# Kernel tuning notes

Measured on AMD Instinct MI355X. Metric: run time of the kernel, lower is better.

## Reference

```python
import jax, jax.numpy as jnp
import numpy as np

E = 1024      # embed_dim
H = 16        # num_heads
HD = E // H   # head_dim = 64
R = 8         # dora rank
T, B = 2048, 2


def setup_inputs() -> dict:
    key = jax.random.key(0)
    ks = jax.random.split(key, 16)
    query = jax.random.normal(ks[0], (T, B, E), dtype=jnp.float32)
    kk = jax.random.normal(ks[1], (T, B, E), dtype=jnp.float32)
    vv = jax.random.normal(ks[2], (T, B, E), dtype=jnp.float32)

    def make_dora(k1, k2, k3, k4):
        w = jax.random.normal(k1, (E, E), dtype=jnp.float32) * (E ** -0.5)
        m = jnp.linalg.norm(w)            # magnitude scalar (Frobenius norm)
        V = w / m                          # frozen direction, ||V||_F = 1
        A = jax.random.normal(k2, (R, E), dtype=jnp.float32) * (E ** -0.5)
        Bm = jax.random.normal(k3, (E, R), dtype=jnp.float32) * 0.01
        b = jax.random.normal(k4, (E,), dtype=jnp.float32) * 0.01
        return m, V, A, Bm, b

    mag_q, dir_q, A_q, B_q, bias_q = make_dora(ks[3], ks[4], ks[5], ks[6])
    mag_v, dir_v, A_v, B_v, bias_v = make_dora(ks[7], ks[8], ks[9], ks[10])
    k_w = jax.random.normal(ks[11], (E, E), dtype=jnp.float32) * (E ** -0.5)
    k_b = jax.random.normal(ks[12], (E,), dtype=jnp.float32) * 0.01
    out_w = jax.random.normal(ks[13], (E, E), dtype=jnp.float32) * (E ** -0.5)
    out_b = jax.random.normal(ks[14], (E,), dtype=jnp.float32) * 0.01
    return dict(query=query, key=kk, value=vv,
                mag_q=mag_q, dir_q=dir_q, A_q=A_q, B_q=B_q, bias_q=bias_q,
                mag_v=mag_v, dir_v=dir_v, A_v=A_v, B_v=B_v, bias_v=bias_v,
                k_w=k_w, k_b=k_b, out_w=out_w, out_b=out_b)


def _dora_linear(x, m, V, A, Bm, b):
    # W_eff = m * (V + B@A) / (||V + B@A||_F + 1e-8); out = x @ W_eff.T + b
    Vu = V + Bm @ A                      # [E, E]
    W = (m / (jnp.linalg.norm(Vu) + 1e-8)) * Vu
    return x @ W.T + b


def reference(query, key, value, mag_q, dir_q, A_q, B_q, bias_q,
              mag_v, dir_v, A_v, B_v, bias_v, k_w, k_b, out_w, out_b):
    # NOTE: source module ignores `key`/`value` and derives k, v from `query`.
    Tq, Bq, _ = query.shape
    q = _dora_linear(query, mag_q, dir_q, A_q, B_q, bias_q)   # [T, B, E]
    k = query @ k_w.T + k_b                                    # frozen K proj
    v = _dora_linear(query, mag_v, dir_v, A_v, B_v, bias_v)
    # (T, B, E) -> (B*H, T, HD), matching torch reshape/transpose
    q = q.reshape(Tq, Bq * H, HD).transpose(1, 0, 2)
    k = k.reshape(Tq, Bq * H, HD).transpose(1, 0, 2)
    v = v.reshape(Tq, Bq * H, HD).transpose(1, 0, 2)
    scale = HD ** -0.5
    attn = jnp.einsum('nqd,nkd->nqk', q, k) * scale            # [B*H, T, T]
    attn = jax.nn.softmax(attn, axis=-1)                       # dropout p=0
    out = jnp.einsum('nqk,nkd->nqd', attn, v)                  # [B*H, T, HD]
    out = out.transpose(1, 0, 2).reshape(Tq, Bq, E)
    out = out @ out_w.T + out_b
    return out
```

## Files before the change

### kernel.cpp

```cpp
#include <hip/hip_runtime.h>
#include <hip/hip_bf16.h>

#define E_DIM 1024
#define T_DIM 2048
#define B_DIM 2
#define H_DIM 16
#define HD_DIM 64
#define R_DIM 8
#define M_ROWS (T_DIM * B_DIM)
#define LOG2E 1.4426950408889634f

typedef __attribute__((ext_vector_type(8))) short bf16x8;
typedef __attribute__((ext_vector_type(4))) short bf16x4;
typedef __attribute__((ext_vector_type(4))) float f32x4;
typedef __attribute__((ext_vector_type(2))) unsigned uint2v;

#if __has_builtin(__builtin_amdgcn_exp2f)
#define EXP2F(x) __builtin_amdgcn_exp2f(x)
#else
#define EXP2F(x) exp2f(x)
#endif

__device__ __forceinline__ unsigned short f2bf(float f) {
  unsigned int u = __builtin_bit_cast(unsigned int, f);
  u += 0x7FFFu + ((u >> 16) & 1u);
  return (unsigned short)(u >> 16);
}

__device__ __forceinline__ unsigned cvt_pk_bf16(float lo, float hi) {
  unsigned r;
  asm("v_cvt_pk_bf16_f32 %0, %1, %2" : "=v"(r) : "v"(lo), "v"(hi));
  return r;
}

__device__ __forceinline__ f32x4 mfma16(bf16x4 a, bf16x4 b, f32x4 c) {
#if __has_builtin(__builtin_amdgcn_mfma_f32_16x16x16bf16_1k)
  return __builtin_amdgcn_mfma_f32_16x16x16bf16_1k(a, b, c, 0, 0, 0);
#elif __has_builtin(__builtin_amdgcn_mfma_f32_16x16x16_bf16)
  return __builtin_amdgcn_mfma_f32_16x16x16_bf16(a, b, c, 0, 0, 0);
#else
  asm("v_mfma_f32_16x16x16_bf16 %0, %1, %2, %0" : "+v"(c) : "v"(a), "v"(b));
  return c;
#endif
}

__device__ __forceinline__ void glds16(const unsigned short* g, unsigned short* l) {
  __builtin_amdgcn_global_load_lds(
      (__attribute__((address_space(1))) void*)(g),
      (__attribute__((address_space(3))) void*)(l), 16, 0, 0);
}

__global__ __launch_bounds__(256) void prep(
    const float* __restrict__ query, const float* __restrict__ k_w,
    const float* __restrict__ out_w,
    const float* __restrict__ dir_q, const float* __restrict__ A_q, const float* __restrict__ B_q,
    const float* __restrict__ dir_v, const float* __restrict__ A_v, const float* __restrict__ B_v,
    unsigned short* __restrict__ qA_bf, unsigned short* __restrict__ kw_bf,
    unsigned short* __restrict__ ow_bf,
    unsigned short* __restrict__ Wq, unsigned short* __restrict__ Wv,
    float* __restrict__ partials) {
  const int bid = blockIdx.x;
  if (bid < 6144) {
    int u = bid * 256 + threadIdx.x;
    const float* src;
    unsigned short* dst;
    if (u < 1048576) { src = query; dst = qA_bf; }
    else if (u < 1310720) { src = k_w; dst = kw_bf; u -= 1048576; }
    else { src = out_w; dst = ow_bf; u -= 1310720; }
    float4 f = reinterpret_cast<const float4*>(src)[u];
    ushort4 o;
    o.x = f2bf(f.x); o.y = f2bf(f.y); o.z = f2bf(f.z); o.w = f2bf(f.w);
    reinterpret_cast<ushort4*>(dst)[u] = o;
    return;
  }
  const int bid2 = bid - 6144;
  const int mat = bid2 >> 8, bx = bid2 & 255;
  const float* __restrict__ dir = mat ? dir_v : dir_q;
  const float* __restrict__ Am  = mat ? A_v   : A_q;
  const float* __restrict__ Bm  = mat ? B_v   : B_q;
  unsigned short* __restrict__ W = mat ? Wv : Wq;

  float sum = 0.0f;
  for (int idx = bx * 256 + threadIdx.x; idx < E_DIM * E_DIM; idx += 256 * 256) {
    int i = idx >> 10;
    int j = idx & (E_DIM - 1);
    float v = dir[idx];
#pragma unroll
    for (int r = 0; r < R_DIM; ++r)
      v += Bm[i * R_DIM + r] * Am[r * E_DIM + j];
    W[idx] = f2bf(v);
    sum += v * v;
  }
#pragma unroll
  for (int off = 32; off > 0; off >>= 1) sum += __shfl_down(sum, off);
  __shared__ float red[4];
  if ((threadIdx.x & 63) == 0) red[threadIdx.x >> 6] = sum;
  __syncthreads();
  if (threadIdx.x == 0)
    partials[mat * 256 + bx] = (red[0] + red[1]) + (red[2] + red[3]);
}

template <int OUT_MODE>
__device__ __forceinline__ void gemm_bt_core(
    const unsigned short* __restrict__ A, const unsigned short* __restrict__ W,
    const float* __restrict__ bias, float scale, float bscale,
    void* __restrict__ Cptr, int bm, int bn) {
  __shared__ unsigned short As[128 * 32];
  __shared__ unsigned short Bs[128 * 32];
  const int tid = threadIdx.x;
  const int w = tid >> 6, lane = tid & 63;
  const int lr = lane & 15, lg = lane >> 4;
  const int wm = w >> 1, wn = w & 1;

  f32x4 acc[4][4];
#pragma unroll
  for (int i = 0; i < 4; ++i)
#pragma unroll
    for (int j = 0; j < 4; ++j) acc[i][j] = (f32x4){0.f, 0.f, 0.f, 0.f};

  const int c0u = tid, c1u = 256 + tid;
  const int r0 = c0u >> 2, o0 = (c0u & 3) * 8;
  const int r1 = c1u >> 2, o1 = (c1u & 3) * 8;

  for (int k0 = 0; k0 < E_DIM; k0 += 32) {
    glds16(A + (size_t)(bm + r0) * E_DIM + k0 + o0, As + c0u * 8);
    glds16(W + (size_t)(bn + r0) * E_DIM + k0 + o0, Bs + c0u * 8);
    glds16(A + (size_t)(bm + r1) * E_DIM + k0 + o1, As + c1u * 8);
    glds16(W + (size_t)(bn + r1) * E_DIM + k0 + o1, Bs + c1u * 8);
    __syncthreads();

    bf16x8 af[4], bf[4];
#pragma unroll
    for (int i = 0; i < 4; ++i)
      af[i] = *reinterpret_cast<const bf16x8*>(As + (wm * 64 + i * 16 + lr) * 32 + lg * 8);
#pragma unroll
    for (int j = 0; j < 4; ++j)
      bf[j] = *reinterpret_cast<const bf16x8*>(Bs + (wn * 64 + j * 16 + lr) * 32 + lg * 8);
#pragma unroll
    for (int i = 0; i < 4; ++i)
#pragma unroll
      for (int j = 0; j < 4; ++j)
        acc[i][j] = __builtin_amdgcn_mfma_f32_16x16x32_bf16(af[i], bf[j], acc[i][j], 0, 0, 0);
    __syncthreads();
  }

  if (OUT_MODE == 2) {
#pragma unroll
    for (int i = 0; i < 4; ++i) {
      int rowbase = bm + wm * 64 + i * 16 + lg * 4;
      float4 bb = *reinterpret_cast<const float4*>(&bias[rowbase]);
      float bbv[4] = {bb.x, bb.y, bb.z, bb.w};
#pragma unroll
      for (int j = 0; j < 4; ++j) {
        int xrow = bn + wn * 64 + j * 16 + lr;
        int t = xrow >> 1, bsel = xrow & 1;
#pragma unroll
        for (int rr = 0; rr < 4; ++rr) {
          int wrow = rowbase + rr;
          float v = scale * acc[i][j][rr] + bbv[rr];
          int nn = (bsel << 4) | (wrow >> 6);
          int d = wrow & 63;
          reinterpret_cast<unsigned short*>(Cptr)[((size_t)nn * HD_DIM + d) * T_DIM + t] = f2bf(v);
        }
      }
    }
  } else {
#pragma unroll
    for (int i = 0; i < 4; ++i) {
      int row = bm + wm * 64 + i * 16 + lg * 4;
#pragma unroll
      for (int j = 0; j < 4; ++j) {
        int col = bn + wn * 64 + j * 16 + lr;
        float bv = bias[col] * bscale;
#pragma unroll
        for (int r = 0; r < 4; ++r) {
          float v = scale * acc[i][j][r] + bv;
          reinterpret_cast<unsigned short*>(Cptr)[(size_t)(row + r) * E_DIM + col] = f2bf(v);
        }
      }
    }
  }
}

__global__ __launch_bounds__(256) void gemm_qkv(
    const unsigned short* __restrict__ Abf,
    const unsigned short* __restrict__ Wq, const unsigned short* __restrict__ Wk,
    const unsigned short* __restrict__ Wv,
    const float* __restrict__ bias_q, const float* __restrict__ k_b,
    const float* __restrict__ bias_v,
    const float* __restrict__ partials, const float* __restrict__ mag_q,
    const float* __restrict__ mag_v,
    unsigned short* __restrict__ qbuf, unsigned short* __restrict__ kbuf,
    unsigned short* __restrict__ vT) {
  const int bid = blockIdx.x;
  const int swz = (bid & 7) * 96 + (bid >> 3);
  const int mat = (swz < 256) ? 0 : (swz < 512) ? 1 : 2;

  float scale = 1.0f, bscale = 1.0f;
  if (mat != 1) {
    const int sel = (mat == 0) ? 0 : 1;
    float s = partials[sel * 256 + threadIdx.x];
#pragma unroll
    for (int off = 32; off > 0; off >>= 1) s += __shfl_down(s, off);
    __shared__ float red[4];
    if ((threadIdx.x & 63) == 0) red[threadIdx.x >> 6] = s;
    __syncthreads();
    float tot = (red[0] + red[1]) + (red[2] + red[3]);
    float m = (mat == 0) ? mag_q[0] : mag_v[0];
    float sc = m / (sqrtf(tot) + 1e-8f);
    if (mat == 0) {
      const float sm = 0.125f * LOG2E;
      scale = sc * sm; bscale = sm;
    } else {
      scale = sc;
    }
    __syncthreads();
  }

  if (mat == 0) {
    const int idx = swz;
    gemm_bt_core<1>(Abf, Wq, bias_q, scale, bscale, qbuf,
                    (idx >> 3) * 128, (idx & 7) * 128);
  } else if (mat == 1) {
    const int idx = swz - 256;
    gemm_bt_core<1>(Abf, Wk, k_b, 1.0f, 1.0f, kbuf,
                    (idx >> 3) * 128, (idx & 7) * 128);
  } else {
    const int idx = swz - 512;
    gemm_bt_core<2>(Wv, Abf, bias_v, scale, 1.0f, vT,
                    (idx >> 5) * 128, (idx & 31) * 128);
  }
}

__global__ __launch_bounds__(256) void gemm_out(
    const unsigned short* __restrict__ Abf, const unsigned short* __restrict__ Wo,
    const float* __restrict__ bias, float* __restrict__ out) {
  const int bid = blockIdx.x;
  const int swz = (bid & 7) * 32 + (bid >> 3);
  const int bm = (swz >> 3) * 128, bn = (swz & 7) * 128;

  __shared__ unsigned short As[128 * 32];
  __shared__ unsigned short Bs[128 * 32];
  const int tid = threadIdx.x;
  const int w = tid >> 6, lane = tid & 63;
  const int lr = lane & 15, lg = lane >> 4;
  const int wm = w >> 1, wn = w & 1;

  f32x4 acc[4][4];
#pragma unroll
  for (int i = 0; i < 4; ++i)
#pragma unroll
    for (int j = 0; j < 4; ++j) acc[i][j] = (f32x4){0.f, 0.f, 0.f, 0.f};

  const int c0u = tid, c1u = 256 + tid;
  const int r0 = c0u >> 2, o0 = (c0u & 3) * 8;
  const int r1 = c1u >> 2, o1 = (c1u & 3) * 8;

  float4 ra0, ra1, rb0, rb1;
  ra0 = *reinterpret_cast<const float4*>(Abf + (size_t)(bm + r0) * E_DIM + o0);
  ra1 = *reinterpret_cast<const float4*>(Abf + (size_t)(bm + r1) * E_DIM + o1);
  rb0 = *reinterpret_cast<const float4*>(Wo + (size_t)(bn + r0) * E_DIM + o0);
  rb1 = *reinterpret_cast<const float4*>(Wo + (size_t)(bn + r1) * E_DIM + o1);

  for (int k0 = 0; k0 < E_DIM; k0 += 32) {
    __syncthreads();
    *reinterpret_cast<float4*>(As + c0u * 8) = ra0;
    *reinterpret_cast<float4*>(As + c1u * 8) = ra1;
    *reinterpret_cast<float4*>(Bs + c0u * 8) = rb0;
    *reinterpret_cast<float4*>(Bs + c1u * 8) = rb1;
    __syncthreads();
    if (k0 + 32 < E_DIM) {
      ra0 = *reinterpret_cast<const float4*>(Abf + (size_t)(bm + r0) * E_DIM + k0 + 32 + o0);
      ra1 = *reinterpret_cast<const float4*>(Abf + (size_t)(bm + r1) * E_DIM + k0 + 32 + o1);
      rb0 = *reinterpret_cast<const float4*>(Wo + (size_t)(bn + r0) * E_DIM + k0 + 32 + o0);
      rb1 = *reinterpret_cast<const float4*>(Wo + (size_t)(bn + r1) * E_DIM + k0 + 32 + o1);
    }

    bf16x8 af[4], bf[4];
#pragma unroll
    for (int i = 0; i < 4; ++i)
      af[i] = *reinterpret_cast<const bf16x8*>(As + (wm * 64 + i * 16 + lr) * 32 + lg * 8);
#pragma unroll
    for (int j = 0; j < 4; ++j)
      bf[j] = *reinterpret_cast<const bf16x8*>(Bs + (wn * 64 + j * 16 + lr) * 32 + lg * 8);
#pragma unroll
    for (int i = 0; i < 4; ++i)
#pragma unroll
      for (int j = 0; j < 4; ++j)
        acc[i][j] = __builtin_amdgcn_mfma_f32_16x16x32_bf16(af[i], bf[j], acc[i][j], 0, 0, 0);
  }

#pragma unroll
  for (int i = 0; i < 4; ++i) {
    int row = bm + wm * 64 + i * 16 + lg * 4;
#pragma unroll
    for (int j = 0; j < 4; ++j) {
      int col = bn + wn * 64 + j * 16 + lr;
      float bv = bias[col];
#pragma unroll
      for (int r = 0; r < 4; ++r)
        out[(size_t)(row + r) * E_DIM + col] = acc[i][j][r] + bv;
    }
  }
}

#define LDPK 72
#define LDPV 136

__global__ __launch_bounds__(512, 2) void attn_mfma(
    const unsigned short* __restrict__ qb, const unsigned short* __restrict__ kb,
    const unsigned short* __restrict__ vT, unsigned short* __restrict__ ob) {
  __shared__ unsigned short Ks2[128 * LDPK];
  __shared__ unsigned short Vt2[64 * LDPV];
  const int n = blockIdx.x, b = n >> 4, col0 = (n & 15) * HD_DIM;
  const int tid = threadIdx.x, w = tid >> 6, lane = tid & 63;
  const int lr = lane & 15, lg = lane >> 4;
  const int q0 = blockIdx.y * 256 + w * 32;

  bf16x8 qf[2][2];
#pragma unroll
  for (int rf = 0; rf < 2; ++rf)
#pragma unroll
    for (int ks = 0; ks < 2; ++ks)
      qf[rf][ks] = *reinterpret_cast<const bf16x8*>(
          qb + ((size_t)(q0 + rf * 16 + lr) * B_DIM + b) * E_DIM + col0 + ks * 32 + lg * 8);

  f32x4 accO[2][4];
#pragma unroll
  for (int rf = 0; rf < 2; ++rf)
#pragma unroll
    for (int df = 0; df < 4; ++df) accO[rf][df] = (f32x4){0.f, 0.f, 0.f, 0.f};
  float mrun0 = -1e30f, mrun1 = -1e30f, lrun0 = 0.f, lrun1 = 0.f;

  const int kr0 = tid >> 3, kc0 = (tid & 7) * 8;
  const int kr1 = 64 + kr0;
  const int vd0 = tid >> 4, vc0 = (tid & 15) * 8;
  const int vd1 = 32 + vd0;
  float4 rk0, rk1, rv0, rv1;
  rk0 = *reinterpret_cast<const float4*>(kb + ((size_t)kr0 * B_DIM + b) * E_DIM + col0 + kc0);
  rk1 = *reinterpret_cast<const float4*>(kb + ((size_t)kr1 * B_DIM + b) * E_DIM + col0 + kc0);
  rv0 = *reinterpret_cast<const float4*>(vT + ((size_t)n * HD_DIM + vd0) * T_DIM + vc0);
  rv1 = *reinterpret_cast<const float4*>(vT + ((size_t)n * HD_DIM + vd1) * T_DIM + vc0);

  for (int kt = 0; kt < T_DIM; kt += 128) {
    __syncthreads();
    *reinterpret_cast<float4*>(Ks2 + kr0 * LDPK + kc0) = rk0;
    *reinterpret_cast<float4*>(Ks2 + kr1 * LDPK + kc0) = rk1;
    *reinterpret_cast<float4*>(Vt2 + vd0 * LDPV + vc0) = rv0;
    *reinterpret_cast<float4*>(Vt2 + vd1 * LDPV + vc0) = rv1;
    __syncthreads();
    if (kt + 128 < T_DIM) {
      int kt2 = kt + 128;
      rk0 = *reinterpret_cast<const float4*>(kb + ((size_t)(kt2 + kr0) * B_DIM + b) * E_DIM + col0 + kc0);
      rk1 = *reinterpret_cast<const float4*>(kb + ((size_t)(kt2 + kr1) * B_DIM + b) * E_DIM + col0 + kc0);
      rv0 = *reinterpret_cast<const float4*>(vT + ((size_t)n * HD_DIM + vd0) * T_DIM + kt2 + vc0);
      rv1 = *reinterpret_cast<const float4*>(vT + ((size_t)n * HD_DIM + vd1) * T_DIM + kt2 + vc0);
    }

#pragma unroll
    for (int h = 0; h < 2; ++h) {
      const unsigned short* Kh = Ks2 + h * 64 * LDPK;
      const unsigned short* Vh = Vt2 + h * 64;

      f32x4 s[4][2];
#pragma unroll
      for (int kf = 0; kf < 4; ++kf)
#pragma unroll
        for (int rf = 0; rf < 2; ++rf) s[kf][rf] = (f32x4){0.f, 0.f, 0.f, 0.f};
      __builtin_amdgcn_s_setprio(1);
#pragma unroll
      for (int ks = 0; ks < 2; ++ks)
#pragma unroll
        for (int kf = 0; kf < 4; ++kf) {
          bf16x8 kfr = *reinterpret_cast<const bf16x8*>(Kh + (kf * 16 + lr) * LDPK + ks * 32 + lg * 8);
#pragma unroll
          for (int rf = 0; rf < 2; ++rf)
            s[kf][rf] = __builtin_amdgcn_mfma_f32_16x16x32_bf16(kfr, qf[rf][ks], s[kf][rf], 0, 0, 0);
        }
      __builtin_amdgcn_s_setprio(0);

      float pm0, pm1;
      {
        float a0 = fmaxf(fmaxf(s[0][0][0], s[0][0][1]), fmaxf(s[0][0][2], s[0][0][3]));
        float a1 = fmaxf(fmaxf(s[1][0][0], s[1][0][1]), fmaxf(s[1][0][2], s[1][0][3]));
        float a2 = fmaxf(fmaxf(s[2][0][0], s[2][0][1]), fmaxf(s[2][0][2], s[2][0][3]));
        float a3 = fmaxf(fmaxf(s[3][0][0], s[3][0][1]), fmaxf(s[3][0][2], s[3][0][3]));
        pm0 = fmaxf(fmaxf(a0, a1), fmaxf(a2, a3));
        float b0 = fmaxf(fmaxf(s[0][1][0], s[0][1][1]), fmaxf(s[0][1][2], s[0][1][3]));
        float b1 = fmaxf(fmaxf(s[1][1][0], s[1][1][1]), fmaxf(s[1][1][2], s[1][1][3]));
        float b2 = fmaxf(fmaxf(s[2][1][0], s[2][1][1]), fmaxf(s[2][1][2], s[2][1][3]));
        float b3 = fmaxf(fmaxf(s[3][1][0], s[3][1][1]), fmaxf(s[3][1][2], s[3][1][3]));
        pm1 = fmaxf(fmaxf(b0, b1), fmaxf(b2, b3));
      }
      pm0 = fmaxf(pm0, __shfl_xor(pm0, 16)); pm0 = fmaxf(pm0, __shfl_xor(pm0, 32));
      pm1 = fmaxf(pm1, __shfl_xor(pm1, 16)); pm1 = fmaxf(pm1, __shfl_xor(pm1, 32));

      const int resc = __any((pm0 > mrun0 + 8.0f) || (pm1 > mrun1 + 8.0f));
      float mn0 = mrun0, mn1 = mrun1;
      if (resc) { mn0 = fmaxf(mn0, pm0); mn1 = fmaxf(mn1, pm1); }

#pragma unroll
      for (int kf = 0; kf < 4; ++kf)
#pragma unroll
        for (int r = 0; r < 4; ++r) {
          s[kf][0][r] = EXP2F(s[kf][0][r] - mn0);
          s[kf][1][r] = EXP2F(s[kf][1][r] - mn1);
        }

      bf16x4 pa4[2][4];
#pragma unroll
      for (int rf = 0; rf < 2; ++rf)
#pragma unroll
        for (int kf = 0; kf < 4; ++kf) {
          uint2v u = (uint2v){cvt_pk_bf16(s[kf][rf][0], s[kf][rf][1]),
                              cvt_pk_bf16(s[kf][rf][2], s[kf][rf][3])};
          pa4[rf][kf] = __builtin_bit_cast(bf16x4, u);
        }

      f32x4 u0 = (s[0][0] + s[1][0]) + (s[2][0] + s[3][0]);
      f32x4 u1 = (s[0][1] + s[1][1]) + (s[2][1] + s[3][1]);
      float ps0 = (u0[0] + u0[1]) + (u0[2] + u0[3]);
      float ps1 = (u1[0] + u1[1]) + (u1[2] + u1[3]);
      ps0 += __shfl_xor(ps0, 16); ps0 += __shfl_xor(ps0, 32);
      ps1 += __shfl_xor(ps1, 16); ps1 += __shfl_xor(ps1, 32);

      if (resc) {
        float al0 = EXP2F(mrun0 - mn0), al1 = EXP2F(mrun1 - mn1);
        mrun0 = mn0; mrun1 = mn1;
        lrun0 = lrun0 * al0 + ps0; lrun1 = lrun1 * al1 + ps1;
#pragma unroll
        for (int r = 0; r < 4; ++r) {
          float a0 = __shfl(al0, (lg << 2) | r);
          float a1 = __shfl(al1, (lg << 2) | r);
#pragma unroll
          for (int df = 0; df < 4; ++df) { accO[0][df][r] *= a0; accO[1][df][r] *= a1; }
        }
      } else {
        lrun0 += ps0; lrun1 += ps1;
      }

      __builtin_amdgcn_s_setprio(1);
#pragma unroll
      for (int kf = 0; kf < 4; ++kf) {
#pragma unroll
        for (int df = 0; df < 4; ++df) {
          bf16x4 vf4 = *reinterpret_cast<const bf16x4*>(
              Vh + (df * 16 + lr) * LDPV + kf * 16 + lg * 4);
          accO[0][df] = mfma16(pa4[0][kf], vf4, accO[0][df]);
          accO[1][df] = mfma16(pa4[1][kf], vf4, accO[1][df]);
        }
      }
      __builtin_amdgcn_s_setprio(0);
    }
  }

#pragma unroll
  for (int rf = 0; rf < 2; ++rf)
#pragma unroll
    for (int r = 0; r < 4; ++r) {
      float lv = __shfl(rf ? lrun1 : lrun0, (lg << 2) | r);
      float inv = 1.0f / lv;
      int row = q0 + rf * 16 + lg * 4 + r;
      size_t base = ((size_t)row * B_DIM + b) * E_DIM + col0;
#pragma unroll
      for (int df = 0; df < 4; ++df)
        ob[base + df * 16 + lr] = f2bf(accO[rf][df][r] * inv);
    }
}

extern "C" void kernel_launch(void* const* d_in, const int* in_sizes, int n_in,
                              void* d_out, int out_size, void* d_ws, size_t ws_size,
                              hipStream_t stream) {
  const float* query  = (const float*)d_in[0];
  const float* mag_q  = (const float*)d_in[3];
  const float* dir_q  = (const float*)d_in[4];
  const float* A_q    = (const float*)d_in[5];
  const float* B_q    = (const float*)d_in[6];
  const float* bias_q = (const float*)d_in[7];
  const float* mag_v  = (const float*)d_in[8];
  const float* dir_v  = (const float*)d_in[9];
  const float* A_v    = (const float*)d_in[10];
  const float* B_v    = (const float*)d_in[11];
  const float* bias_v = (const float*)d_in[12];
  const float* k_w    = (const float*)d_in[13];
  const float* k_b    = (const float*)d_in[14];
  const float* out_w  = (const float*)d_in[15];
  const float* out_b  = (const float*)d_in[16];
  float* out = (float*)d_out;

  char* ws = (char*)d_ws;
  float* partials = (float*)ws;
  unsigned short* qA_bf = (unsigned short*)(ws + 4096);
  unsigned short* wq_bf = qA_bf + (size_t)M_ROWS * E_DIM;
  unsigned short* wv_bf = wq_bf + (size_t)E_DIM * E_DIM;
  unsigned short* kw_bf = wv_bf + (size_t)E_DIM * E_DIM;
  unsigned short* ow_bf = kw_bf + (size_t)E_DIM * E_DIM;
  unsigned short* qbuf  = ow_bf + (size_t)E_DIM * E_DIM;
  unsigned short* kbuf  = qbuf + (size_t)M_ROWS * E_DIM;
  unsigned short* vTbuf = kbuf + (size_t)M_ROWS * E_DIM;
  unsigned short* abuf  = vTbuf + (size_t)M_ROWS * E_DIM;

  prep<<<6656, 256, 0, stream>>>(query, k_w, out_w,
                                 dir_q, A_q, B_q, dir_v, A_v, B_v,
                                 qA_bf, kw_bf, ow_bf, wq_bf, wv_bf, partials);

  gemm_qkv<<<768, 256, 0, stream>>>(qA_bf, wq_bf, kw_bf, wv_bf,
                                    bias_q, k_b, bias_v,
                                    partials, mag_q, mag_v,
                                    qbuf, kbuf, vTbuf);
  attn_mfma<<<dim3(B_DIM * H_DIM, T_DIM / 256), 512, 0, stream>>>(
      qbuf, kbuf, vTbuf, abuf);
  gemm_out<<<256, 256, 0, stream>>>(abuf, ow_bf, out_b, out);
}
```

Before: 153.3 us.

## Fuse Q and K projections into one tile loop sharing the A-tile loads

The Q and K projection GEMMs now run in the same block. Each k-step loads the activation tile into LDS once and multiplies it against both the Wq and Wk tiles, keeping two accumulator sets. This halves the activation reads for these two matrices and cuts the grid from 768 to 512 blocks. In exchange each thread holds twice as many accumulators, which raises register pressure, and launch_bounds(256,2) is added to try to keep two blocks per CU.

```diff
diff --git a/kernel.cpp b/kernel.cpp
--- a/kernel.cpp
+++ b/kernel.cpp
@@ -182,7 +182,7 @@
   }
 }
 
-__global__ __launch_bounds__(256) void gemm_qkv(
+__global__ __launch_bounds__(256, 2) void gemm_qkv(
     const unsigned short* __restrict__ Abf,
     const unsigned short* __restrict__ Wq, const unsigned short* __restrict__ Wk,
     const unsigned short* __restrict__ Wv,
@@ -193,42 +193,99 @@
     unsigned short* __restrict__ qbuf, unsigned short* __restrict__ kbuf,
     unsigned short* __restrict__ vT) {
   const int bid = blockIdx.x;
-  const int swz = (bid & 7) * 96 + (bid >> 3);
-  const int mat = (swz < 256) ? 0 : (swz < 512) ? 1 : 2;
-
-  float scale = 1.0f, bscale = 1.0f;
-  if (mat != 1) {
-    const int sel = (mat == 0) ? 0 : 1;
-    float s = partials[sel * 256 + threadIdx.x];
+  const int swz = (bid & 7) * 64 + (bid >> 3);
+  const int tid = threadIdx.x;
+
+  if (swz >= 256) {
+    float s = partials[256 + tid];
 #pragma unroll
     for (int off = 32; off > 0; off >>= 1) s += __shfl_down(s, off);
-    __shared__ float red[4];
-    if ((threadIdx.x & 63) == 0) red[threadIdx.x >> 6] = s;
-    __syncthreads();
-    float tot = (red[0] + red[1]) + (red[2] + red[3]);
-    float m = (mat == 0) ? mag_q[0] : mag_v[0];
-    float sc = m / (sqrtf(tot) + 1e-8f);
-    if (mat == 0) {
-      const float sm = 0.125f * LOG2E;
-      scale = sc * sm; bscale = sm;
-    } else {
-      scale = sc;
-    }
-    __syncthreads();
-  }
-
-  if (mat == 0) {
-    const int idx = swz;
-    gemm_bt_core<1>(Abf, Wq, bias_q, scale, bscale, qbuf,
-                    (idx >> 3) * 128, (idx & 7) * 128);
-  } else if (mat == 1) {
+    __shared__ float redv[4];
+    if ((tid & 63) == 0) redv[tid >> 6] = s;
+    __syncthreads();
+    float tot = (redv[0] + redv[1]) + (redv[2] + redv[3]);
+    float scale = mag_v[0] / (sqrtf(tot) + 1e-8f);
+    __syncthreads();
     const int idx = swz - 256;
-    gemm_bt_core<1>(Abf, Wk, k_b, 1.0f, 1.0f, kbuf,
-                    (idx >> 3) * 128, (idx & 7) * 128);
-  } else {
-    const int idx = swz - 512;
     gemm_bt_core<2>(Wv, Abf, bias_v, scale, 1.0f, vT,
                     (idx >> 5) * 128, (idx & 31) * 128);
+    return;
+  }
+
+  float s = partials[tid];
+#pragma unroll
+  for (int off = 32; off > 0; off >>= 1) s += __shfl_down(s, off);
+  __shared__ float red[4];
+  if ((tid & 63) == 0) red[tid >> 6] = s;
+  __syncthreads();
+  float tot = (red[0] + red[1]) + (red[2] + red[3]);
+  const float sm = 0.125f * LOG2E;
+  const float qscale = (mag_q[0] / (sqrtf(tot) + 1e-8f)) * sm;
+  __syncthreads();
+
+  const int bm = (swz >> 3) * 128, bn = (swz & 7) * 128;
+  __shared__ unsigned short As[128 * 32];
+  __shared__ unsigned short Bqs[128 * 32];
+  __shared__ unsigned short Bks[128 * 32];
+  const int w = tid >> 6, lane = tid & 63;
+  const int lr = lane & 15, lg = lane >> 4;
+  const int wm = w >> 1, wn = w & 1;
+
+  f32x4 accq[4][4], acck[4][4];
+#pragma unroll
+  for (int i = 0; i < 4; ++i)
+#pragma unroll
+    for (int j = 0; j < 4; ++j) {
+      accq[i][j] = (f32x4){0.f, 0.f, 0.f, 0.f};
+      acck[i][j] = (f32x4){0.f, 0.f, 0.f, 0.f};
+    }
+
+  const int c0u = tid, c1u = 256 + tid;
+  const int r0 = c0u >> 2, o0 = (c0u & 3) * 8;
+  const int r1 = c1u >> 2, o1 = (c1u & 3) * 8;
+
+  for (int k0 = 0; k0 < E_DIM; k0 += 32) {
+    glds16(Abf + (size_t)(bm + r0) * E_DIM + k0 + o0, As + c0u * 8);
+    glds16(Abf + (size_t)(bm + r1) * E_DIM + k0 + o1, As + c1u * 8);
+    glds16(Wq + (size_t)(bn + r0) * E_DIM + k0 + o0, Bqs + c0u * 8);
+    glds16(Wq + (size_t)(bn + r1) * E_DIM + k0 + o1, Bqs + c1u * 8);
+    glds16(Wk + (size_t)(bn + r0) * E_DIM + k0 + o0, Bks + c0u * 8);
+    glds16(Wk + (size_t)(bn + r1) * E_DIM + k0 + o1, Bks + c1u * 8);
+    __syncthreads();
+
+    bf16x8 af[4], bq[4], bk[4];
+#pragma unroll
+    for (int i = 0; i < 4; ++i)
+      af[i] = *reinterpret_cast<const bf16x8*>(As + (wm * 64 + i * 16 + lr) * 32 + lg * 8);
+#pragma unroll
+    for (int j = 0; j < 4; ++j) {
+      bq[j] = *reinterpret_cast<const bf16x8*>(Bqs + (wn * 64 + j * 16 + lr) * 32 + lg * 8);
+      bk[j] = *reinterpret_cast<const bf16x8*>(Bks + (wn * 64 + j * 16 + lr) * 32 + lg * 8);
+    }
+#pragma unroll
+    for (int i = 0; i < 4; ++i)
+#pragma unroll
+      for (int j = 0; j < 4; ++j) {
+        accq[i][j] = __builtin_amdgcn_mfma_f32_16x16x32_bf16(af[i], bq[j], accq[i][j], 0, 0, 0);
+        acck[i][j] = __builtin_amdgcn_mfma_f32_16x16x32_bf16(af[i], bk[j], acck[i][j], 0, 0, 0);
+      }
+    __syncthreads();
+  }
+
+#pragma unroll
+  for (int i = 0; i < 4; ++i) {
+    int row = bm + wm * 64 + i * 16 + lg * 4;
+#pragma unroll
+    for (int j = 0; j < 4; ++j) {
+      int col = bn + wn * 64 + j * 16 + lr;
+      float bq_ = bias_q[col] * sm;
+      float bk_ = k_b[col];
+#pragma unroll
+      for (int r = 0; r < 4; ++r) {
+        qbuf[(size_t)(row + r) * E_DIM + col] = f2bf(qscale * accq[i][j][r] + bq_);
+        kbuf[(size_t)(row + r) * E_DIM + col] = f2bf(acck[i][j][r] + bk_);
+      }
+    }
   }
 }
 
@@ -504,7 +561,7 @@
                                  dir_q, A_q, B_q, dir_v, A_v, B_v,
                                  qA_bf, kw_bf, ow_bf, wq_bf, wv_bf, partials);
 
-  gemm_qkv<<<768, 256, 0, stream>>>(qA_bf, wq_bf, kw_bf, wv_bf,
+  gemm_qkv<<<512, 256, 0, stream>>>(qA_bf, wq_bf, kw_bf, wv_bf,
                                     bias_q, k_b, bias_v,
                                     partials, mag_q, mag_v,
                                     qbuf, kbuf, vTbuf);
```

After: 144.8 us, median of 2. 5.5% less time.
